# Performance work log

Hardware: AMD Instinct MI355X
Metric: run time of the kernel (lower is better)

## Reference

```python
import jax, jax.numpy as jnp
import numpy as np

D_MODEL = 1024
N_HEADS = 16
D_HEAD = D_MODEL // N_HEADS
IGNORE = -100000.0


def setup_inputs() -> dict:
    key = jax.random.key(0)
    ks = jax.random.split(key, 12)
    B, S = 4, 2048
    x_q = jax.random.normal(ks[0], (B, S, D_MODEL), dtype=jnp.float32)
    x_kv = jax.random.normal(ks[1], (B, S, D_MODEL), dtype=jnp.float32)
    # mask[q, k] == True means the score is replaced with IGNORE (masked out)
    mask = jax.random.randint(ks[2], (S, S), 0, 2) == 1
    sq = 1.0 / np.sqrt(D_MODEL)
    sh = 1.0 / np.sqrt(D_HEAD)
    W_Q = jax.random.normal(ks[3], (N_HEADS, D_MODEL, D_HEAD), dtype=jnp.float32) * sq
    W_K = jax.random.normal(ks[4], (N_HEADS, D_MODEL, D_HEAD), dtype=jnp.float32) * sq
    W_V = jax.random.normal(ks[5], (N_HEADS, D_MODEL, D_HEAD), dtype=jnp.float32) * sq
    W_O = jax.random.normal(ks[6], (N_HEADS, D_HEAD, D_MODEL), dtype=jnp.float32) * sh
    b_Q = jnp.zeros((N_HEADS, D_HEAD), dtype=jnp.float32)
    b_K = jnp.zeros((N_HEADS, D_HEAD), dtype=jnp.float32)
    b_V = jnp.zeros((N_HEADS, D_HEAD), dtype=jnp.float32)
    b_O = jnp.zeros((D_MODEL,), dtype=jnp.float32)
    return {"x_q": x_q, "x_kv": x_kv, "mask": mask,
            "W_Q": W_Q, "W_K": W_K, "W_V": W_V, "W_O": W_O,
            "b_Q": b_Q, "b_K": b_K, "b_V": b_V, "b_O": b_O}


def reference(x_q, x_kv, mask, W_Q, W_K, W_V, W_O, b_Q, b_K, b_V, b_O):
    # per-head QKV projections: b s d, n d h -> b s n h
    q = jnp.einsum('bsd,ndh->bsnh', x_q, W_Q) + b_Q
    k = jnp.einsum('bsd,ndh->bsnh', x_kv, W_K) + b_K
    v = jnp.einsum('bsd,ndh->bsnh', x_kv, W_V) + b_V
    scale = 1.0 / np.sqrt(D_HEAD)  # flex_attention default scaling
    # scores: [B, H, Sq, Sk]
    scores = jnp.einsum('bqnh,bknh->bnqk', q, k) * scale
    # score_mod: where mask True -> IGNORE
    scores = jnp.where(mask[None, None, :, :], jnp.float32(IGNORE), scores)
    attn = jax.nn.softmax(scores, axis=-1)
    z = jnp.einsum('bnqk,bknh->bqnh', attn, v)  # [B, Sq, H, Dh]
    # per-head output projection then sum over heads
    out = jnp.einsum('bqnh,nhd->bqd', z, W_O) + b_O
    return (out, z)
```

## Files before the change

kernel.cpp:

```cpp
#include <hip/hip_runtime.h>

#define S_LEN 2048
#define NHEAD 16
#define DHEAD 64
#define DMODEL 1024
#define BATCH 4
#define SC2 0.18033688011112042f

typedef short bf16x8 __attribute__((ext_vector_type(8)));
typedef float f32x4 __attribute__((ext_vector_type(4)));
typedef unsigned short u16;
typedef unsigned short u16x8 __attribute__((ext_vector_type(8)));
typedef unsigned short u16x4 __attribute__((ext_vector_type(4)));
typedef unsigned long long u64;
typedef unsigned long long u64x2 __attribute__((ext_vector_type(2)));

__device__ __forceinline__ u16 f2b(float f) {
  unsigned u = __builtin_bit_cast(unsigned, f);
  u += 0x7FFFu + ((u >> 16) & 1u);
  return (u16)(u >> 16);
}
__device__ __forceinline__ float b2f(u16 v) {
  unsigned u = ((unsigned)v) << 16;
  return __builtin_bit_cast(float, u);
}
__device__ __forceinline__ f32x4 mfma16(bf16x8 a, bf16x8 b, f32x4 c) {
  return __builtin_amdgcn_mfma_f32_16x16x32_bf16(a, b, c, 0, 0, 0);
}
__device__ __forceinline__ void load_lds16(const void* g, void* l) {
  __builtin_amdgcn_global_load_lds(
      (const __attribute__((address_space(1))) unsigned int*)g,
      (__attribute__((address_space(3))) unsigned int*)l, 16, 0, 0);
}
__device__ __forceinline__ float fexp2(float x) {
  float r;
  asm("v_exp_f32 %0, %1\n\ts_nop 1" : "=v"(r) : "v"(x));
  return r;
}
__device__ __forceinline__ unsigned cvtpk(float lo, float hi) {
  unsigned r;
  asm("v_cvt_pk_bf16_f32 %0, %1, %2" : "=v"(r) : "v"(lo), "v"(hi));
  return r;
}


__global__ void cvt_f32_bf16(const float* __restrict__ src, u16* __restrict__ dst, int n4) {
  int i = blockIdx.x * 256 + threadIdx.x;
  int stride = gridDim.x * 256;
  for (; i < n4; i += stride) {
    float4 v = ((const float4*)src)[i];
    u16x4 o = { f2b(v.x), f2b(v.y), f2b(v.z), f2b(v.w) };
    ((u16x4*)dst)[i] = o;
  }
}

__global__ void mask_expand(const int* __restrict__ M, u64* __restrict__ Mex) {
  int idx = blockIdx.x * 256 + threadIdx.x;
  int q = idx >> 9, k = (idx & 511) * 4;
  int4 v = *(const int4*)(M + (size_t)q * S_LEN + k);
  int T = k >> 6, t = (k >> 4) & 3, g = (k >> 2) & 3;
  u64 m = 0;
  if (!v.x) m |= 0xFFFFull;
  if (!v.y) m |= 0xFFFF0000ull;
  if (!v.z) m |= 0xFFFF00000000ull;
  if (!v.w) m |= 0xFFFF000000000000ull;
  Mex[((size_t)q * 32 + T) * 16 + g * 4 + t] = m;
}

__global__ void repack_w(const float* __restrict__ W, u16* __restrict__ WT, float scale) {
  __shared__ u16 t[64][66];
  const int tid = threadIdx.x;
  const int n = blockIdx.y, d0 = blockIdx.x * 64;
  const float* src = W + (size_t)n * 65536;
  for (int p = 0; p < 4; ++p) {
    int idx = p * 256 + tid;
    int r = idx >> 4, cs = idx & 15;
    float4 v = *(const float4*)(src + (size_t)(d0 + r) * 64 + cs * 4);
    t[r][cs*4+0] = f2b(v.x*scale); t[r][cs*4+1] = f2b(v.y*scale);
    t[r][cs*4+2] = f2b(v.z*scale); t[r][cs*4+3] = f2b(v.w*scale);
  }
  __syncthreads();
  for (int p = 0; p < 2; ++p) {
    int idx = p * 256 + tid;
    int hl = idx >> 3, ds = idx & 7;
    u16x8 o;
    for (int e = 0; e < 8; ++e) o[e] = t[ds*8+e][hl];
    *(u16x8*)(WT + (size_t)(n*64 + hl) * 1024 + d0 + ds*8) = o;
  }
}

__global__ void split_wo(const float* __restrict__ Wo, u16* __restrict__ Hi, u16* __restrict__ Lo) {
  __shared__ u16 th[64][66];
  __shared__ u16 tl[64][66];
  const int tid = threadIdx.x;
  const int d0 = blockIdx.x * 64, c0 = blockIdx.y * 64;
  for (int p = 0; p < 4; ++p) {
    int idx = p * 256 + tid;
    int r = idx >> 4, cs = idx & 15;
    float4 v = *(const float4*)(Wo + (size_t)(c0 + r) * 1024 + d0 + cs * 4);
    float f[4] = {v.x, v.y, v.z, v.w};
    for (int e = 0; e < 4; ++e) {
      u16 hb = f2b(f[e]);
      th[r][cs*4+e] = hb;
      tl[r][cs*4+e] = f2b(f[e] - b2f(hb));
    }
  }
  __syncthreads();
  for (int p = 0; p < 2; ++p) {
    int idx = p * 256 + tid;
    int dr = idx >> 3, cs = idx & 7;
    u16x8 oh, ol;
    for (int e = 0; e < 8; ++e) { oh[e] = th[cs*8+e][dr]; ol[e] = tl[cs*8+e][dr]; }
    *(u16x8*)(Hi + (size_t)(d0 + dr) * 1024 + c0 + cs*8) = oh;
    *(u16x8*)(Lo + (size_t)(d0 + dr) * 1024 + c0 + cs*8) = ol;
  }
}

__global__ void transpose_v(const u16* __restrict__ V, u16* __restrict__ VT) {
  __shared__ u16 t[64][66];
  const int tid = threadIdx.x;
  const int s0 = blockIdx.x * 64;
  const int b = blockIdx.y >> 4, h = blockIdx.y & 15;
  for (int p = 0; p < 2; ++p) {
    int idx = p * 256 + tid;
    int r = idx >> 3, sg = idx & 7;
    u16x8 v = *(const u16x8*)(V + (size_t)(b*S_LEN + s0 + r) * 1024 + h*64 + sg*8);
    for (int e = 0; e < 8; ++e) t[r][sg*8+e] = v[e];
  }
  __syncthreads();
  for (int p = 0; p < 2; ++p) {
    int idx = p * 256 + tid;
    int dr = idx >> 3, ss = idx & 7;
    u16x8 o;
    for (int e = 0; e < 8; ++e) o[e] = t[ss*8+e][dr];
    *(u16x8*)(VT + ((size_t)(b*NHEAD + h) * 64 + dr) * 2048 + s0 + ss*8) = o;
  }
}


template<int BF16OUT>
__global__ __launch_bounds__(256, 2)
void gemm_bt(const u16* __restrict__ A, const u16* __restrict__ Bt,
             const float* __restrict__ bias, float bscale, void* __restrict__ Cout)
{
  __shared__ __align__(16) char As[16384];
  __shared__ __align__(16) char Bs[16384];
  const int tid = threadIdx.x, wid = tid >> 6, lane = tid & 63;
  const int lq = lane & 15, g = lane >> 4;
  const size_t am0 = (size_t)blockIdx.y * 128;
  const size_t bn0 = (size_t)blockIdx.x * 128;
  const int wr = (wid >> 1) * 64, wc = (wid & 1) * 64;
  f32x4 z4 = {0.f, 0.f, 0.f, 0.f};
  f32x4 acc[4][4];
  for (int i = 0; i < 4; ++i) for (int j = 0; j < 4; ++j) acc[i][j] = z4;
  for (int k0 = 0; k0 < DMODEL; k0 += 64) {
#pragma unroll
    for (int c = 0; c < 4; ++c) {
      int idx = c*256 + tid, r = idx >> 3, s = idx & 7;
      load_lds16(A + (am0 + r)*DMODEL + k0 + ((s ^ (r & 7)) << 3), As + idx*16);
    }
#pragma unroll
    for (int c = 0; c < 4; ++c) {
      int idx = c*256 + tid, r = idx >> 3, s = idx & 7;
      load_lds16(Bt + (bn0 + r)*DMODEL + k0 + ((s ^ (r & 7)) << 3), Bs + idx*16);
    }
    __syncthreads();
#pragma unroll
    for (int ks = 0; ks < 2; ++ks) {
      bf16x8 af[4], bfr[4];
#pragma unroll
      for (int i = 0; i < 4; ++i) {
        int row = wr + i*16 + lq;
        af[i] = *(const bf16x8*)(As + row*128 + (((ks*4 + g) ^ (row & 7)) << 4));
      }
#pragma unroll
      for (int j = 0; j < 4; ++j) {
        int row = wc + j*16 + lq;
        bfr[j] = *(const bf16x8*)(Bs + row*128 + (((ks*4 + g) ^ (row & 7)) << 4));
      }
#pragma unroll
      for (int i = 0; i < 4; ++i)
#pragma unroll
        for (int j = 0; j < 4; ++j)
          acc[i][j] = mfma16(af[i], bfr[j], acc[i][j]);
    }
    __syncthreads();
  }
#pragma unroll
  for (int i = 0; i < 4; ++i)
#pragma unroll
    for (int j = 0; j < 4; ++j) {
      size_t row = am0 + wr + i*16 + g*4;
      int col = (int)bn0 + wc + j*16 + lq;
      float bv = bias[col] * bscale;
#pragma unroll
      for (int r = 0; r < 4; ++r) {
        float v = acc[i][j][r] + bv;
        if (BF16OUT) ((u16*)Cout)[(row + r)*DMODEL + col] = f2b(v);
        else         ((float*)Cout)[(row + r)*DMODEL + col] = v;
      }
    }
}


__global__ __launch_bounds__(256, 2)
void gemm_out(const float* __restrict__ Z, const u16* __restrict__ Bh,
              const u16* __restrict__ Bl, const float* __restrict__ bias,
              float* __restrict__ Cout)
{
  __shared__ __align__(16) char Ah[16384];
  __shared__ __align__(16) char Al[16384];
  __shared__ __align__(16) char Bhs[16384];
  __shared__ __align__(16) char Bls[16384];
  const int tid = threadIdx.x, wid = tid >> 6, lane = tid & 63;
  const int lq = lane & 15, g = lane >> 4;
  const size_t am0 = (size_t)blockIdx.y * 128;
  const size_t bn0 = (size_t)blockIdx.x * 128;
  const int wr = (wid >> 1) * 64, wc = (wid & 1) * 64;
  f32x4 z4 = {0.f, 0.f, 0.f, 0.f};
  f32x4 acc[4][4];
  for (int i = 0; i < 4; ++i) for (int j = 0; j < 4; ++j) acc[i][j] = z4;
  for (int k0 = 0; k0 < DMODEL; k0 += 64) {
#pragma unroll
    for (int c = 0; c < 8; ++c) {
      int idx = c*256 + tid, r = idx >> 4, fs = idx & 15;
      float4 v = *(const float4*)(Z + (am0 + r)*DMODEL + k0 + fs*4);
      float f[4] = {v.x, v.y, v.z, v.w};
      u16x4 hv, lv;
      for (int e = 0; e < 4; ++e) {
        u16 hb = f2b(f[e]);
        hv[e] = hb;
        lv[e] = f2b(f[e] - b2f(hb));
      }
      int byo = r*128 + ((((fs >> 1) ^ (r & 7)) << 4) | ((fs & 1) << 3));
      *(u16x4*)(Ah + byo) = hv;
      *(u16x4*)(Al + byo) = lv;
    }
#pragma unroll
    for (int c = 0; c < 4; ++c) {
      int idx = c*256 + tid, r = idx >> 3, s = idx & 7;
      load_lds16(Bh + (bn0 + r)*DMODEL + k0 + ((s ^ (r & 7)) << 3), Bhs + idx*16);
    }
#pragma unroll
    for (int c = 0; c < 4; ++c) {
      int idx = c*256 + tid, r = idx >> 3, s = idx & 7;
      load_lds16(Bl + (bn0 + r)*DMODEL + k0 + ((s ^ (r & 7)) << 3), Bls + idx*16);
    }
    __syncthreads();
#pragma unroll
    for (int ks = 0; ks < 2; ++ks) {
      bf16x8 ah[4], al[4], bh4[4], bl4[4];
#pragma unroll
      for (int i = 0; i < 4; ++i) {
        int row = wr + i*16 + lq;
        int off = row*128 + (((ks*4 + g) ^ (row & 7)) << 4);
        ah[i] = *(const bf16x8*)(Ah + off);
        al[i] = *(const bf16x8*)(Al + off);
      }
#pragma unroll
      for (int j = 0; j < 4; ++j) {
        int row = wc + j*16 + lq;
        int off = row*128 + (((ks*4 + g) ^ (row & 7)) << 4);
        bh4[j] = *(const bf16x8*)(Bhs + off);
        bl4[j] = *(const bf16x8*)(Bls + off);
      }
#pragma unroll
      for (int i = 0; i < 4; ++i)
#pragma unroll
        for (int j = 0; j < 4; ++j) {
          acc[i][j] = mfma16(al[i], bh4[j], acc[i][j]);
          acc[i][j] = mfma16(ah[i], bl4[j], acc[i][j]);
          acc[i][j] = mfma16(ah[i], bh4[j], acc[i][j]);
        }
    }
    __syncthreads();
  }
#pragma unroll
  for (int i = 0; i < 4; ++i)
#pragma unroll
    for (int j = 0; j < 4; ++j) {
      size_t row = am0 + wr + i*16 + g*4;
      int col = (int)bn0 + wc + j*16 + lq;
      float bv = bias[col];
#pragma unroll
      for (int r = 0; r < 4; ++r)
        Cout[(row + r)*DMODEL + col] = acc[i][j][r] + bv;
    }
}

__global__ __launch_bounds__(256, 3)
void attn(const u16* __restrict__ Q, const u16* __restrict__ K,
          const u16* __restrict__ VT, const u64* __restrict__ Mex,
          float* __restrict__ Zf)
{
  __shared__ __align__(16) char L[49152];
  const int tid = threadIdx.x, wid = tid >> 6, lane = tid & 63;
  const int lq = lane & 15, g = lane >> 4;
  const int Lb = blockIdx.x;
  const int xcd = Lb & 7, slot = Lb >> 3;
  const int qt = slot & 15, pl = slot >> 4;
  const int pair = xcd * 8 + pl;
  const int h = pair & 15, b = pair >> 4;
  const int q0 = qt * 128;
  const int qw = q0 + wid * 32;

  bf16x8 qf[2][2];
#pragma unroll
  for (int u = 0; u < 2; ++u) {
    const u16* qp = Q + (size_t)(b*S_LEN + qw + u*16 + lq) * DMODEL + h*DHEAD + g*8;
    qf[u][0] = *(const bf16x8*)qp;
    qf[u][1] = *(const bf16x8*)(qp + 32);
  }
  bf16x8 ones;
#pragma unroll
  for (int e = 0; e < 8; ++e) ones[e] = (short)0x3F80;

  const f32x4 z4 = {0.f, 0.f, 0.f, 0.f};
  f32x4 Oc[2][4];
#pragma unroll
  for (int u = 0; u < 2; ++u)
#pragma unroll
    for (int t = 0; t < 4; ++t) Oc[u][t] = z4;
  f32x4 lrow[2] = {z4, z4};

  const u16* kp = K + (size_t)(b*S_LEN)*DMODEL + h*DHEAD;
  const u16* vp = VT + (size_t)((b*NHEAD + h)*DHEAD)*S_LEN;
  const u64* mx0 = Mex + (size_t)(qw + lq) * 512 + g*4;
  const u64* mx1 = Mex + (size_t)(qw + 16 + lq) * 512 + g*4;
  char* myP = L + 32768 + wid*4096;

  size_t ko[2], vo[2];
  int sd[2];
#pragma unroll
  for (int c = 0; c < 2; ++c) {
    int idx = c*256 + tid, r = idx >> 3, s = idx & 7, so = (s ^ (r & 7)) << 3;
    ko[c] = (size_t)r * DMODEL + so;
    vo[c] = (size_t)r * S_LEN + so;
    sd[c] = idx * 16;
  }

  bf16x8 kr0, kr1, vr0, vr1;
  kr0 = *(const bf16x8*)(kp + ko[0]); kr1 = *(const bf16x8*)(kp + ko[1]);
  vr0 = *(const bf16x8*)(vp + vo[0]); vr1 = *(const bf16x8*)(vp + vo[1]);
  u64x2 m0a = *(const u64x2*)(mx0), m0b = *(const u64x2*)(mx0 + 2);
  u64x2 m1a = *(const u64x2*)(mx1), m1b = *(const u64x2*)(mx1 + 2);
  kp += 64*DMODEL; vp += 64;
  *(bf16x8*)(L + sd[0]) = kr0;  *(bf16x8*)(L + sd[1]) = kr1;
  *(bf16x8*)(L + 8192 + sd[0]) = vr0;  *(bf16x8*)(L + 8192 + sd[1]) = vr1;
  __syncthreads();

  for (int it = 0; it < 32; ++it) {
    char* Bu = L + (it & 1) * 16384;
    char* Bn = L + ((it + 1) & 1) * 16384;
    u64x2 n0a = {0,0}, n0b = {0,0}, n1a = {0,0}, n1b = {0,0};
    if (it < 31) {
      kr0 = *(const bf16x8*)(kp + ko[0]); kr1 = *(const bf16x8*)(kp + ko[1]);
      vr0 = *(const bf16x8*)(vp + vo[0]); vr1 = *(const bf16x8*)(vp + vo[1]);
      n0a = *(const u64x2*)(mx0 + (it+1)*16);
      n0b = *(const u64x2*)(mx0 + (it+1)*16 + 2);
      n1a = *(const u64x2*)(mx1 + (it+1)*16);
      n1b = *(const u64x2*)(mx1 + (it+1)*16 + 2);
      kp += 64*DMODEL; vp += 64;
    }

    f32x4 st[2][4];
    __builtin_amdgcn_s_setprio(1);
#pragma unroll
    for (int t = 0; t < 4; ++t) {
      int row = t*16 + lq;
      bf16x8 kf0 = *(const bf16x8*)(Bu + row*128 + ((g ^ (row & 7)) << 4));
      bf16x8 kf1 = *(const bf16x8*)(Bu + row*128 + (((4 + g) ^ (row & 7)) << 4));
      st[0][t] = mfma16(kf1, qf[0][1], mfma16(kf0, qf[0][0], z4));
      st[1][t] = mfma16(kf1, qf[1][1], mfma16(kf0, qf[1][0], z4));
    }
    __builtin_amdgcn_s_setprio(0);

#pragma unroll
    for (int u = 0; u < 2; ++u) {
      char* pb = myP + (u*16 + lq) * 128;
#pragma unroll
      for (int t = 0; t < 4; ++t) {
        int sl = (((t*2 + (g >> 1)) ^ (lq & 7)) << 4) + ((g & 1) << 3);
        float p0 = fexp2(st[u][t][0]);
        float p1 = fexp2(st[u][t][1]);
        float p2 = fexp2(st[u][t][2]);
        float p3 = fexp2(st[u][t][3]);
        u64 mt = u ? ((t < 2) ? m1a[t & 1] : m1b[t & 1])
                   : ((t < 2) ? m0a[t & 1] : m0b[t & 1]);
        union { unsigned w32[2]; u64 w64; } pw;
        pw.w32[0] = cvtpk(p0, p1);
        pw.w32[1] = cvtpk(p2, p3);
        *(u64*)(pb + sl) = pw.w64 & mt;
      }
    }
    asm volatile("s_waitcnt lgkmcnt(0)" ::: "memory");
    __builtin_amdgcn_sched_barrier(0);

    bf16x8 pf[2][2];
#pragma unroll
    for (int u = 0; u < 2; ++u) {
      char* pb = myP + (u*16 + lq) * 128;
      pf[u][0] = *(const bf16x8*)(pb + (((0 + g) ^ (lq & 7)) << 4));
      pf[u][1] = *(const bf16x8*)(pb + (((4 + g) ^ (lq & 7)) << 4));
    }

    __builtin_amdgcn_s_setprio(1);
    f32x4 ts0 = mfma16(pf[0][1], ones, mfma16(pf[0][0], ones, z4));
    f32x4 ts1 = mfma16(pf[1][1], ones, mfma16(pf[1][0], ones, z4));
#pragma unroll
    for (int t = 0; t < 4; ++t) {
      int row = t*16 + lq;
#pragma unroll
      for (int hh = 0; hh < 2; ++hh) {
        bf16x8 vf = *(const bf16x8*)(Bu + 8192 + row*128 + (((hh*4 + g) ^ (row & 7)) << 4));
        Oc[0][t] = mfma16(pf[0][hh], vf, Oc[0][t]);
        Oc[1][t] = mfma16(pf[1][hh], vf, Oc[1][t]);
      }
    }
    __builtin_amdgcn_s_setprio(0);
    lrow[0] += ts0;
    lrow[1] += ts1;

    if (it < 31) {
      *(bf16x8*)(Bn + sd[0]) = kr0;  *(bf16x8*)(Bn + sd[1]) = kr1;
      *(bf16x8*)(Bn + 8192 + sd[0]) = vr0;  *(bf16x8*)(Bn + 8192 + sd[1]) = vr1;
    }
    __syncthreads();
    m0a = n0a; m0b = n0b; m1a = n1a; m1b = n1b;
  }

#pragma unroll
  for (int u = 0; u < 2; ++u) {
    float i0 = 1.f / lrow[u][0], i1 = 1.f / lrow[u][1],
          i2 = 1.f / lrow[u][2], i3 = 1.f / lrow[u][3];
#pragma unroll
    for (int t = 0; t < 4; ++t) {
      size_t base = ((size_t)(b*S_LEN + qw + u*16 + g*4) * NHEAD + h) * DHEAD + t*16 + lq;
      Zf[base       ] = Oc[u][t][0] * i0;
      Zf[base + 1024] = Oc[u][t][1] * i1;
      Zf[base + 2048] = Oc[u][t][2] * i2;
      Zf[base + 3072] = Oc[u][t][3] * i3;
    }
  }
}


extern "C" void kernel_launch(void* const* d_in, const int* in_sizes, int n_in,
                              void* d_out, int out_size, void* d_ws, size_t ws_size,
                              hipStream_t stream) {
  const float* x_q  = (const float*)d_in[0];
  const float* x_kv = (const float*)d_in[1];
  const int*   mask = (const int*)d_in[2];
  const float* W_Q  = (const float*)d_in[3];
  const float* W_K  = (const float*)d_in[4];
  const float* W_V  = (const float*)d_in[5];
  const float* W_O  = (const float*)d_in[6];
  const float* b_Q  = (const float*)d_in[7];
  const float* b_K  = (const float*)d_in[8];
  const float* b_V  = (const float*)d_in[9];
  const float* b_O  = (const float*)d_in[10];

  if (ws_size < 102760448) return;

  u16* ws  = (u16*)d_ws;
  u16* XQ  = ws;
  u16* XKV = XQ  + 8388608;
  u16* WQT = XKV + 8388608;
  u16* WKT = WQT + 1048576;
  u16* WVT = WKT + 1048576;
  u16* WOH = WVT + 1048576;
  u16* WOL = WOH + 1048576;
  u16* Qb  = WOL + 1048576;
  u16* Kb  = Qb  + 8388608;
  u16* Vb  = Kb  + 8388608;
  u64* Mxp = (u64*)(Vb + 8388608);
  u16* VTp = XQ;

  float* out = (float*)d_out;
  float* zf  = out + 8388608;

  cvt_f32_bf16<<<2048, 256, 0, stream>>>(x_q,  XQ,  2097152);
  cvt_f32_bf16<<<2048, 256, 0, stream>>>(x_kv, XKV, 2097152);
  repack_w<<<dim3(16,16), 256, 0, stream>>>(W_Q, WQT, SC2);
  repack_w<<<dim3(16,16), 256, 0, stream>>>(W_K, WKT, 1.0f);
  repack_w<<<dim3(16,16), 256, 0, stream>>>(W_V, WVT, 1.0f);
  split_wo<<<dim3(16,16), 256, 0, stream>>>(W_O, WOH, WOL);
  mask_expand<<<4096, 256, 0, stream>>>(mask, Mxp);
  gemm_bt<1><<<dim3(8,64), 256, 0, stream>>>(XQ,  WQT, b_Q, SC2, Qb);
  gemm_bt<1><<<dim3(8,64), 256, 0, stream>>>(XKV, WKT, b_K, 1.0f, Kb);
  gemm_bt<1><<<dim3(8,64), 256, 0, stream>>>(XKV, WVT, b_V, 1.0f, Vb);
  transpose_v<<<dim3(32,64), 256, 0, stream>>>(Vb, VTp);
  attn<<<1024, 256, 0, stream>>>(Qb, Kb, VTp, Mxp, zf);
  gemm_out<<<dim3(8,64), 256, 0, stream>>>(zf, WOH, WOL, b_O, out);
}
```

Measured before the change: 283.1 us.

## Merge prep and QKV launches, split Z into bf16 hi/lo inside attention

Merges the two input conversions and the mask expansion into one prepass kernel, the three weight repacks into one launch, and the three QKV GEMMs into one z-indexed launch, cutting launch count and tail effects. The attention epilogue now also writes Z as bf16 hi/lo halves, so the output GEMM can stream them into LDS with async global-to-LDS loads instead of converting fp32 in registers. The exp2 calls are grouped into one asm block with a single shared nop. This adds extra scattered 2-byte stores in the attention epilogue and reuses the XKV and Vb workspace buffers for the Z halves.

```diff
diff --git a/kernel.cpp b/kernel.cpp
--- a/kernel.cpp
+++ b/kernel.cpp
@@ -32,10 +32,13 @@
       (const __attribute__((address_space(1))) unsigned int*)g,
       (__attribute__((address_space(3))) unsigned int*)l, 16, 0, 0);
 }
-__device__ __forceinline__ float fexp2(float x) {
-  float r;
-  asm("v_exp_f32 %0, %1\n\ts_nop 1" : "=v"(r) : "v"(x));
-  return r;
+__device__ __forceinline__ void fexp2x4(float& a, float& b, float& c, float& d) {
+  asm("v_exp_f32 %0, %0\n\t"
+      "v_exp_f32 %1, %1\n\t"
+      "v_exp_f32 %2, %2\n\t"
+      "v_exp_f32 %3, %3\n\t"
+      "s_nop 1"
+      : "+v"(a), "+v"(b), "+v"(c), "+v"(d));
 }
 __device__ __forceinline__ unsigned cvtpk(float lo, float hi) {
   unsigned r;
@@ -44,31 +47,48 @@
 }
 
 
-__global__ void cvt_f32_bf16(const float* __restrict__ src, u16* __restrict__ dst, int n4) {
+__global__ void prepass(const float* __restrict__ xq, const float* __restrict__ xkv,
+                        const int* __restrict__ M,
+                        u16* __restrict__ XQ, u16* __restrict__ XKV,
+                        u64* __restrict__ Mex)
+{
   int i = blockIdx.x * 256 + threadIdx.x;
   int stride = gridDim.x * 256;
-  for (; i < n4; i += stride) {
-    float4 v = ((const float4*)src)[i];
-    u16x4 o = { f2b(v.x), f2b(v.y), f2b(v.z), f2b(v.w) };
-    ((u16x4*)dst)[i] = o;
-  }
-}
-
-__global__ void mask_expand(const int* __restrict__ M, u64* __restrict__ Mex) {
-  int idx = blockIdx.x * 256 + threadIdx.x;
-  int q = idx >> 9, k = (idx & 511) * 4;
-  int4 v = *(const int4*)(M + (size_t)q * S_LEN + k);
-  int T = k >> 6, t = (k >> 4) & 3, g = (k >> 2) & 3;
-  u64 m = 0;
-  if (!v.x) m |= 0xFFFFull;
-  if (!v.y) m |= 0xFFFF0000ull;
-  if (!v.z) m |= 0xFFFF00000000ull;
-  if (!v.w) m |= 0xFFFF000000000000ull;
-  Mex[((size_t)q * 32 + T) * 16 + g * 4 + t] = m;
-}
-
-__global__ void repack_w(const float* __restrict__ W, u16* __restrict__ WT, float scale) {
+  for (; i < 5242880; i += stride) {
+    if (i < 2097152) {
+      float4 v = ((const float4*)xq)[i];
+      u16x4 o = { f2b(v.x), f2b(v.y), f2b(v.z), f2b(v.w) };
+      ((u16x4*)XQ)[i] = o;
+    } else if (i < 4194304) {
+      int j = i - 2097152;
+      float4 v = ((const float4*)xkv)[j];
+      u16x4 o = { f2b(v.x), f2b(v.y), f2b(v.z), f2b(v.w) };
+      ((u16x4*)XKV)[j] = o;
+    } else {
+      int idx = i - 4194304;
+      int q = idx >> 9, k = (idx & 511) * 4;
+      int4 v = *(const int4*)(M + (size_t)q * S_LEN + k);
+      int T = k >> 6, t = (k >> 4) & 3, g = (k >> 2) & 3;
+      u64 m = 0;
+      if (!v.x) m |= 0xFFFFull;
+      if (!v.y) m |= 0xFFFF0000ull;
+      if (!v.z) m |= 0xFFFF00000000ull;
+      if (!v.w) m |= 0xFFFF000000000000ull;
+      Mex[((size_t)q * 32 + T) * 16 + g * 4 + t] = m;
+    }
+  }
+}
+
+__global__ void repack_w3(const float* __restrict__ WQ, const float* __restrict__ WK,
+                          const float* __restrict__ WV,
+                          u16* __restrict__ WQT, u16* __restrict__ WKT,
+                          u16* __restrict__ WVT)
+{
   __shared__ u16 t[64][66];
+  const int which = blockIdx.z;
+  const float* W = which == 0 ? WQ : (which == 1 ? WK : WV);
+  u16* WT = which == 0 ? WQT : (which == 1 ? WKT : WVT);
+  const float scale = which == 0 ? SC2 : 1.0f;
   const int tid = threadIdx.x;
   const int n = blockIdx.y, d0 = blockIdx.x * 64;
   const float* src = W + (size_t)n * 65536;
@@ -138,11 +158,21 @@
 }
 
 
-template<int BF16OUT>
 __global__ __launch_bounds__(256, 2)
-void gemm_bt(const u16* __restrict__ A, const u16* __restrict__ Bt,
-             const float* __restrict__ bias, float bscale, void* __restrict__ Cout)
+void gemm_qkv(const u16* __restrict__ XQ, const u16* __restrict__ XKV,
+              const u16* __restrict__ WQT, const u16* __restrict__ WKT,
+              const u16* __restrict__ WVT,
+              const float* __restrict__ bQ, const float* __restrict__ bK,
+              const float* __restrict__ bV,
+              u16* __restrict__ Qb, u16* __restrict__ Kb, u16* __restrict__ Vb)
 {
+  const int which = blockIdx.z;
+  const u16* A  = which == 0 ? XQ : XKV;
+  const u16* Bt = which == 0 ? WQT : (which == 1 ? WKT : WVT);
+  const float* bias = which == 0 ? bQ : (which == 1 ? bK : bV);
+  const float bscale = which == 0 ? SC2 : 1.0f;
+  u16* Cout = which == 0 ? Qb : (which == 1 ? Kb : Vb);
+
   __shared__ __align__(16) char As[16384];
   __shared__ __align__(16) char Bs[16384];
   const int tid = threadIdx.x, wid = tid >> 6, lane = tid & 63;
@@ -194,19 +224,16 @@
       int col = (int)bn0 + wc + j*16 + lq;
       float bv = bias[col] * bscale;
 #pragma unroll
-      for (int r = 0; r < 4; ++r) {
-        float v = acc[i][j][r] + bv;
-        if (BF16OUT) ((u16*)Cout)[(row + r)*DMODEL + col] = f2b(v);
-        else         ((float*)Cout)[(row + r)*DMODEL + col] = v;
-      }
+      for (int r = 0; r < 4; ++r)
+        Cout[(row + r)*DMODEL + col] = f2b(acc[i][j][r] + bv);
     }
 }
 
 
 __global__ __launch_bounds__(256, 2)
-void gemm_out(const float* __restrict__ Z, const u16* __restrict__ Bh,
-              const u16* __restrict__ Bl, const float* __restrict__ bias,
-              float* __restrict__ Cout)
+void gemm_out(const u16* __restrict__ Zh, const u16* __restrict__ Zl,
+              const u16* __restrict__ Bh, const u16* __restrict__ Bl,
+              const float* __restrict__ bias, float* __restrict__ Cout)
 {
   __shared__ __align__(16) char Ah[16384];
   __shared__ __align__(16) char Al[16384];
@@ -222,29 +249,13 @@
   for (int i = 0; i < 4; ++i) for (int j = 0; j < 4; ++j) acc[i][j] = z4;
   for (int k0 = 0; k0 < DMODEL; k0 += 64) {
 #pragma unroll
-    for (int c = 0; c < 8; ++c) {
-      int idx = c*256 + tid, r = idx >> 4, fs = idx & 15;
-      float4 v = *(const float4*)(Z + (am0 + r)*DMODEL + k0 + fs*4);
-      float f[4] = {v.x, v.y, v.z, v.w};
-      u16x4 hv, lv;
-      for (int e = 0; e < 4; ++e) {
-        u16 hb = f2b(f[e]);
-        hv[e] = hb;
-        lv[e] = f2b(f[e] - b2f(hb));
-      }
-      int byo = r*128 + ((((fs >> 1) ^ (r & 7)) << 4) | ((fs & 1) << 3));
-      *(u16x4*)(Ah + byo) = hv;
-      *(u16x4*)(Al + byo) = lv;
-    }
-#pragma unroll
     for (int c = 0; c < 4; ++c) {
       int idx = c*256 + tid, r = idx >> 3, s = idx & 7;
-      load_lds16(Bh + (bn0 + r)*DMODEL + k0 + ((s ^ (r & 7)) << 3), Bhs + idx*16);
-    }
-#pragma unroll
-    for (int c = 0; c < 4; ++c) {
-      int idx = c*256 + tid, r = idx >> 3, s = idx & 7;
-      load_lds16(Bl + (bn0 + r)*DMODEL + k0 + ((s ^ (r & 7)) << 3), Bls + idx*16);
+      int so = (s ^ (r & 7)) << 3;
+      load_lds16(Zh + (am0 + r)*DMODEL + k0 + so, Ah + idx*16);
+      load_lds16(Zl + (am0 + r)*DMODEL + k0 + so, Al + idx*16);
+      load_lds16(Bh + (bn0 + r)*DMODEL + k0 + so, Bhs + idx*16);
+      load_lds16(Bl + (bn0 + r)*DMODEL + k0 + so, Bls + idx*16);
     }
     __syncthreads();
 #pragma unroll
@@ -291,7 +302,7 @@
 __global__ __launch_bounds__(256, 3)
 void attn(const u16* __restrict__ Q, const u16* __restrict__ K,
           const u16* __restrict__ VT, const u64* __restrict__ Mex,
-          float* __restrict__ Zf)
+          float* __restrict__ Zf, u16* __restrict__ Zh, u16* __restrict__ Zl)
 {
   __shared__ __align__(16) char L[49152];
   const int tid = threadIdx.x, wid = tid >> 6, lane = tid & 63;
@@ -381,10 +392,9 @@
 #pragma unroll
       for (int t = 0; t < 4; ++t) {
         int sl = (((t*2 + (g >> 1)) ^ (lq & 7)) << 4) + ((g & 1) << 3);
-        float p0 = fexp2(st[u][t][0]);
-        float p1 = fexp2(st[u][t][1]);
-        float p2 = fexp2(st[u][t][2]);
-        float p3 = fexp2(st[u][t][3]);
+        float p0 = st[u][t][0], p1 = st[u][t][1];
+        float p2 = st[u][t][2], p3 = st[u][t][3];
+        fexp2x4(p0, p1, p2, p3);
         u64 mt = u ? ((t < 2) ? m1a[t & 1] : m1b[t & 1])
                    : ((t < 2) ? m0a[t & 1] : m0b[t & 1]);
         union { unsigned w32[2]; u64 w64; } pw;
@@ -436,10 +446,15 @@
 #pragma unroll
     for (int t = 0; t < 4; ++t) {
       size_t base = ((size_t)(b*S_LEN + qw + u*16 + g*4) * NHEAD + h) * DHEAD + t*16 + lq;
-      Zf[base       ] = Oc[u][t][0] * i0;
-      Zf[base + 1024] = Oc[u][t][1] * i1;
-      Zf[base + 2048] = Oc[u][t][2] * i2;
-      Zf[base + 3072] = Oc[u][t][3] * i3;
+      float zv[4] = { Oc[u][t][0]*i0, Oc[u][t][1]*i1, Oc[u][t][2]*i2, Oc[u][t][3]*i3 };
+#pragma unroll
+      for (int r = 0; r < 4; ++r) {
+        size_t off = base + (size_t)r * 1024;
+        Zf[off] = zv[r];
+        u16 hb = f2b(zv[r]);
+        Zh[off] = hb;
+        Zl[off] = f2b(zv[r] - b2f(hb));
+      }
     }
   }
 }
@@ -475,21 +490,18 @@
   u16* Vb  = Kb  + 8388608;
   u64* Mxp = (u64*)(Vb + 8388608);
   u16* VTp = XQ;
+  u16* Zh  = XKV;
+  u16* Zl  = Vb;
 
   float* out = (float*)d_out;
   float* zf  = out + 8388608;
 
-  cvt_f32_bf16<<<2048, 256, 0, stream>>>(x_q,  XQ,  2097152);
-  cvt_f32_bf16<<<2048, 256, 0, stream>>>(x_kv, XKV, 2097152);
-  repack_w<<<dim3(16,16), 256, 0, stream>>>(W_Q, WQT, SC2);
-  repack_w<<<dim3(16,16), 256, 0, stream>>>(W_K, WKT, 1.0f);
-  repack_w<<<dim3(16,16), 256, 0, stream>>>(W_V, WVT, 1.0f);
+  prepass<<<4096, 256, 0, stream>>>(x_q, x_kv, mask, XQ, XKV, Mxp);
+  repack_w3<<<dim3(16,16,3), 256, 0, stream>>>(W_Q, W_K, W_V, WQT, WKT, WVT);
   split_wo<<<dim3(16,16), 256, 0, stream>>>(W_O, WOH, WOL);
-  mask_expand<<<4096, 256, 0, stream>>>(mask, Mxp);
-  gemm_bt<1><<<dim3(8,64), 256, 0, stream>>>(XQ,  WQT, b_Q, SC2, Qb);
-  gemm_bt<1><<<dim3(8,64), 256, 0, stream>>>(XKV, WKT, b_K, 1.0f, Kb);
-  gemm_bt<1><<<dim3(8,64), 256, 0, stream>>>(XKV, WVT, b_V, 1.0f, Vb);
+  gemm_qkv<<<dim3(8,64,3), 256, 0, stream>>>(XQ, XKV, WQT, WKT, WVT,
+                                             b_Q, b_K, b_V, Qb, Kb, Vb);
   transpose_v<<<dim3(32,64), 256, 0, stream>>>(Vb, VTp);
-  attn<<<1024, 256, 0, stream>>>(Qb, Kb, VTp, Mxp, zf);
-  gemm_out<<<dim3(8,64), 256, 0, stream>>>(zf, WOH, WOL, b_O, out);
-}
+  attn<<<1024, 256, 0, stream>>>(Qb, Kb, VTp, Mxp, zf, Zh, Zl);
+  gemm_out<<<dim3(8,64), 256, 0, stream>>>(Zh, Zl, WOH, WOL, b_O, out);
+}
```

After: 257.5 us. 9.0% less time.
